# Performance work log

Measured on AMD Instinct MI355X. Metric: run time of the kernel, lower is better.

## Reference

```python
import jax, jax.numpy as jnp
import numpy as np

N = 10000
E = 160000
NEG_SLOPE = 0.2  # PyG GATConv default leaky_relu slope


def _gat_layer(x, src, dst, W, a_src, a_dst, b):
    """PyG GATConv with concat=True, add_self_loops=False.
    x: [N, Fin], W: [Fin, H*C], a_src/a_dst: [H, C], b: [H*C].
    """
    H, C = a_src.shape
    h = (x @ W).reshape(-1, H, C)                      # [N, H, C]
    al_s = jnp.sum(h * a_src, axis=-1)                 # [N, H]
    al_d = jnp.sum(h * a_dst, axis=-1)                 # [N, H]
    e = jax.nn.leaky_relu(al_s[src] + al_d[dst], NEG_SLOPE)  # [E, H]
    # segment softmax over edges grouped by destination node
    m = jax.ops.segment_max(e, dst, num_segments=N)    # [N, H]
    m = jnp.where(jnp.isfinite(m), m, 0.0)
    ex = jnp.exp(e - m[dst])                           # [E, H]
    den = jax.ops.segment_sum(ex, dst, num_segments=N)  # [N, H]
    alpha = ex / jnp.maximum(den[dst], 1e-16)          # [E, H]
    # scatter-add weighted source features
    out = jax.ops.segment_sum(alpha[:, :, None] * h[src], dst, num_segments=N)  # [N, H, C]
    return out.reshape(-1, H * C) + b


def setup_inputs() -> dict:
    key = jax.random.key(0)
    ks = jax.random.split(key, 16)
    s = 0.05
    return {
        "x": jax.random.normal(ks[0], (N, 300), jnp.float32),
        "edge_index": jax.random.randint(ks[1], (2, E), 0, N, jnp.int32),
        "W1": jax.random.normal(ks[2], (300, 512), jnp.float32) * s,
        "att_src1": jax.random.normal(ks[3], (4, 128), jnp.float32) * s,
        "att_dst1": jax.random.normal(ks[4], (4, 128), jnp.float32) * s,
        "b1": jax.random.normal(ks[5], (512,), jnp.float32) * s,
        "Wl1": jax.random.normal(ks[6], (300, 512), jnp.float32) * s,
        "bl1": jax.random.normal(ks[7], (512,), jnp.float32) * s,
        "W2": jax.random.normal(ks[8], (512, 2048), jnp.float32) * s,
        "att_src2": jax.random.normal(ks[9], (4, 512), jnp.float32) * s,
        "att_dst2": jax.random.normal(ks[10], (4, 512), jnp.float32) * s,
        "b2": jax.random.normal(ks[11], (2048,), jnp.float32) * s,
        "Wl2": jax.random.normal(ks[12], (512, 2048), jnp.float32) * s,
        "bl2": jax.random.normal(ks[13], (2048,), jnp.float32) * s,
    }


def reference(x, edge_index, W1, att_src1, att_dst1, b1, Wl1, bl1,
              W2, att_src2, att_dst2, b2, Wl2, bl2):
    src, dst = edge_index[0], edge_index[1]
    h1 = _gat_layer(x, src, dst, W1, att_src1, att_dst1, b1) + (x @ Wl1 + bl1)
    h1 = jax.nn.relu(h1)
    out = _gat_layer(h1, src, dst, W2, att_src2, att_dst2, b2) + (h1 @ Wl2 + bl2)
    return out
```

## Files before the change

### kernel.cpp

```cpp
#include <hip/hip_runtime.h>
#include <hip/hip_bf16.h>
#include <cstdint>


__device__ __forceinline__ float lrelu(float v) { return v >= 0.f ? v : 0.2f * v; }

__device__ __forceinline__ short f2bf(float x) {
  unsigned u = __float_as_uint(x);
  unsigned r = (u + 0x7fffu + ((u >> 16) & 1u)) >> 16;
  return (short)r;
}
__device__ __forceinline__ float bf2f(short b) {
  return __uint_as_float(((unsigned)(unsigned short)b) << 16);
}

typedef __attribute__((ext_vector_type(8))) short bf16x8;
typedef __attribute__((ext_vector_type(4))) float f32x4;

__device__ __forceinline__ void gload_lds16(const void* g, void* l) {
  auto gp = (const __attribute__((address_space(1))) unsigned int*)(uintptr_t)g;
  auto lp = (__attribute__((address_space(3))) unsigned int*)(uintptr_t)l;
  __builtin_amdgcn_global_load_lds(gp, lp, 16, 0, 0);
}

__global__ void count_edges_k(const int* __restrict__ dstv, int* __restrict__ counts, int E) {
  int e = blockIdx.x * 256 + threadIdx.x;
  if (e < E) atomicAdd(&counts[dstv[e]], 1);
}

__global__ void scan_k(const int* __restrict__ counts, int* __restrict__ rowptr,
                       int* __restrict__ cursor, int n) {
  __shared__ int wsum[16];
  __shared__ int s_base;
  int tid = threadIdx.x, lane = tid & 63, wv = tid >> 6;
  if (tid == 0) s_base = 0;
  __syncthreads();
  for (int base = 0; base < n; base += 1024) {
    int i = base + tid;
    int v = (i < n) ? counts[i] : 0;
    int x = v;
#pragma unroll
    for (int off = 1; off < 64; off <<= 1) {
      int t = __shfl_up(x, off);
      if (lane >= off) x += t;
    }
    if (lane == 63) wsum[wv] = x;
    __syncthreads();
    int woff = 0, tot = 0;
#pragma unroll
    for (int w = 0; w < 16; ++w) {
      int s = wsum[w];
      tot += s;
      if (w < wv) woff += s;
    }
    int b = s_base;
    if (i < n) {
      int excl = b + woff + x - v;
      rowptr[i] = excl;
      cursor[i] = excl;
    }
    __syncthreads();
    if (tid == 0) s_base = b + tot;
  }
  __syncthreads();
  if (tid == 0) rowptr[n] = s_base;
}

__global__ void fill_csr_k(const int* __restrict__ srcv, const int* __restrict__ dstv,
                           int* __restrict__ cursor, int* __restrict__ csr_src, int E) {
  int e = blockIdx.x * 256 + threadIdx.x;
  if (e < E) {
    int p = atomicAdd(&cursor[dstv[e]], 1);
    csr_src[p] = srcv[e];
  }
}

__global__ void xsplit_k(const float* __restrict__ x, short* __restrict__ xh,
                         short* __restrict__ xl, int total) {
  int idx = blockIdx.x * 256 + threadIdx.x;
  if (idx >= total) return;
  int n = idx / 320, k = idx - n * 320;
  float v = (k < 300) ? x[(size_t)n * 300 + k] : 0.f;
  short h = f2bf(v);
  xh[idx] = h;
  xl[idx] = f2bf(v - bf2f(h));
}

__global__ void wsplit_t_k(const float* __restrict__ W, short* __restrict__ Wth,
                           short* __restrict__ Wtl, int Nn, int Kin, int Kpad) {
  int idx = blockIdx.x * 256 + threadIdx.x;
  if (idx >= Nn * Kpad) return;
  int n = idx / Kpad, k = idx - n * Kpad;
  float a = (k < Kin) ? W[(size_t)k * Nn + n] : 0.f;
  short h = f2bf(a);
  Wth[idx] = h;
  Wtl[idx] = f2bf(a - bf2f(h));
}

template <bool BIAS>
__global__ __launch_bounds__(256) void gemm_bf16x3_k(
    const short* __restrict__ Ah, const short* __restrict__ Al,
    const short* __restrict__ Bh, const short* __restrict__ Bl,
    const float* __restrict__ bias, float* __restrict__ C,
    int M, int Nn, int K) {
  __shared__ __align__(16) short Ash[128 * 32];
  __shared__ __align__(16) short Asl[128 * 32];
  __shared__ __align__(16) short Bsh[128 * 32];
  __shared__ __align__(16) short Bsl[128 * 32];
  int tid = threadIdx.x, w = tid >> 6, l = tid & 63;
  int m0 = blockIdx.y * 128, n0 = blockIdx.x * 128;
  int wm = (w >> 1) * 64, wn = (w & 1) * 64;

  f32x4 acc[4][4] = {};

  int r_in = l >> 2;
  int kq = (l & 3) * 8;
  int arow_base = m0 + w * 32 + r_in;
  int brow_base = n0 + w * 32 + r_in;
  int lbase = (w * 32) * 32;

  int fr = l & 15, fk = (l >> 4) * 8;

  for (int k0 = 0; k0 < K; k0 += 32) {
    __syncthreads();
#pragma unroll
    for (int i = 0; i < 2; ++i) {
      int am = min(arow_base + i * 16, M - 1);
      int bn = brow_base + i * 16;
      size_t aoff = (size_t)am * K + k0 + kq;
      size_t boff = (size_t)bn * K + k0 + kq;
      int lofs = lbase + i * (16 * 32);
      gload_lds16(Ah + aoff, &Ash[lofs]);
      gload_lds16(Al + aoff, &Asl[lofs]);
      gload_lds16(Bh + boff, &Bsh[lofs]);
      gload_lds16(Bl + boff, &Bsl[lofs]);
    }
    __syncthreads();

    bf16x8 afh[4], afl[4], bfh[4], bfl[4];
#pragma unroll
    for (int t = 0; t < 4; ++t) {
      int ar = wm + t * 16 + fr;
      afh[t] = *(const bf16x8*)&Ash[ar * 32 + fk];
      afl[t] = *(const bf16x8*)&Asl[ar * 32 + fk];
      int br = wn + t * 16 + fr;
      bfh[t] = *(const bf16x8*)&Bsh[br * 32 + fk];
      bfl[t] = *(const bf16x8*)&Bsl[br * 32 + fk];
    }
#pragma unroll
    for (int mi = 0; mi < 4; ++mi)
#pragma unroll
      for (int ni = 0; ni < 4; ++ni) {
        acc[mi][ni] = __builtin_amdgcn_mfma_f32_16x16x32_bf16(afh[mi], bfh[ni], acc[mi][ni], 0, 0, 0);
        acc[mi][ni] = __builtin_amdgcn_mfma_f32_16x16x32_bf16(afh[mi], bfl[ni], acc[mi][ni], 0, 0, 0);
        acc[mi][ni] = __builtin_amdgcn_mfma_f32_16x16x32_bf16(afl[mi], bfh[ni], acc[mi][ni], 0, 0, 0);
      }
  }

  int fq = (l >> 4) * 4;
#pragma unroll
  for (int ni = 0; ni < 4; ++ni) {
    int gc = n0 + wn + ni * 16 + fr;
    float bv = BIAS ? bias[gc] : 0.f;
#pragma unroll
    for (int mi = 0; mi < 4; ++mi) {
      int grb = m0 + wm + mi * 16 + fq;
#pragma unroll
      for (int r = 0; r < 4; ++r) {
        int gr = grb + r;
        if (gr < M) C[(size_t)gr * Nn + gc] = acc[mi][ni][r] + bv;
      }
    }
  }
}

template <int C>
__global__ __launch_bounds__(256) void att_coef_k(
    const float* __restrict__ hfeat, const float* __restrict__ a_src,
    const float* __restrict__ a_dst, float* __restrict__ al_s,
    float* __restrict__ al_d, int n) {
  int wave = threadIdx.x >> 6, lane = threadIdx.x & 63;
  int node = blockIdx.x * 4 + wave;
  if (node >= n) return;
  constexpr int F = 4 * C;
  const float* hrow = hfeat + (size_t)node * F;
  float s[4] = {0, 0, 0, 0}, d[4] = {0, 0, 0, 0};
  for (int f = lane; f < F; f += 64) {
    float hv = hrow[f];
    int h = f / C;
    s[h] = fmaf(hv, a_src[f], s[h]);
    d[h] = fmaf(hv, a_dst[f], d[h]);
  }
#pragma unroll
  for (int off = 32; off; off >>= 1) {
#pragma unroll
    for (int h = 0; h < 4; ++h) {
      s[h] += __shfl_xor(s[h], off);
      d[h] += __shfl_xor(d[h], off);
    }
  }
  if (lane == 0) {
#pragma unroll
    for (int h = 0; h < 4; ++h) {
      al_s[node * 4 + h] = s[h];
      al_d[node * 4 + h] = d[h];
    }
  }
}

__global__ __launch_bounds__(256) void edge_alpha_k(
    const float* __restrict__ al_s, const float* __restrict__ al_d,
    const int* __restrict__ rowptr, const int* __restrict__ csr_src,
    float* __restrict__ alpha, int N) {
  int wave = threadIdx.x >> 6, lane = threadIdx.x & 63;
  int n = blockIdx.x * 4 + wave;
  if (n >= N) return;
  int r0 = rowptr[n], r1 = rowptr[n + 1];
  float ald[4];
#pragma unroll
  for (int h = 0; h < 4; ++h) ald[h] = al_d[n * 4 + h];

  float m[4] = {-3.4e38f, -3.4e38f, -3.4e38f, -3.4e38f};
  for (int e = r0 + lane; e < r1; e += 64) {
    int s = csr_src[e];
#pragma unroll
    for (int h = 0; h < 4; ++h) m[h] = fmaxf(m[h], lrelu(al_s[s * 4 + h] + ald[h]));
  }
#pragma unroll
  for (int off = 32; off; off >>= 1)
#pragma unroll
    for (int h = 0; h < 4; ++h) m[h] = fmaxf(m[h], __shfl_xor(m[h], off));

  float den[4] = {0, 0, 0, 0};
  for (int e = r0 + lane; e < r1; e += 64) {
    int s = csr_src[e];
#pragma unroll
    for (int h = 0; h < 4; ++h) den[h] += expf(lrelu(al_s[s * 4 + h] + ald[h]) - m[h]);
  }
#pragma unroll
  for (int off = 32; off; off >>= 1)
#pragma unroll
    for (int h = 0; h < 4; ++h) den[h] += __shfl_xor(den[h], off);

  float rden[4];
#pragma unroll
  for (int h = 0; h < 4; ++h) rden[h] = 1.f / fmaxf(den[h], 1e-16f);

  for (int e = r0 + lane; e < r1; e += 64) {
    int s = csr_src[e];
#pragma unroll
    for (int h = 0; h < 4; ++h)
      alpha[(size_t)e * 4 + h] = expf(lrelu(al_s[s * 4 + h] + ald[h]) - m[h]) * rden[h];
  }
}

template <int F, int TILE, bool RELU, bool SPLIT>
__global__ __launch_bounds__(256) void spmm_k(
    const float* __restrict__ hfeat, const float* __restrict__ alpha,
    const int* __restrict__ rowptr, const int* __restrict__ csr_src,
    const float* __restrict__ bias, const float* __restrict__ skip,
    float* __restrict__ out, short* __restrict__ oh, short* __restrict__ ol, int N) {
  constexpr int VE = TILE / 64;
  constexpr int C = F / 4;
  int wave = threadIdx.x >> 6, lane = threadIdx.x & 63;
  int n = blockIdx.x * 4 + wave;
  if (n >= N) return;
  int y = blockIdx.y;
  int col = y * TILE + lane * VE;
  int head = (y * TILE) / C;
  int r0 = rowptr[n], r1 = rowptr[n + 1];
  int len = r1 - r0;
  unsigned laneoff = (unsigned)(lane * VE);

  float acc[4][VE] = {};
  for (int base = 0; base < len; base += 64) {
    unsigned sj = 0;
    float aj = 0.f;
    if (base + lane < len) {
      int e = r0 + base + lane;
      sj = (unsigned)csr_src[e] * (unsigned)F + (unsigned)(y * TILE);
      aj = alpha[(size_t)e * 4 + head];
    }
    int cnt = min(64, len - base);
    int j = 0;
    for (; j + 4 <= cnt; j += 4) {
#pragma unroll
      for (int q = 0; q < 4; ++q) {
        unsigned sF = (unsigned)__builtin_amdgcn_readlane((int)sj, j + q);
        float a = __uint_as_float(
            (unsigned)__builtin_amdgcn_readlane((int)__float_as_uint(aj), j + q));
        const float* row = hfeat + sF;
        if (VE == 4) {
          float4 v = *(const float4*)(row + laneoff);
          acc[q][0] = fmaf(a, v.x, acc[q][0]);
          acc[q][1] = fmaf(a, v.y, acc[q][1]);
          acc[q][2] = fmaf(a, v.z, acc[q][2]);
          acc[q][3] = fmaf(a, v.w, acc[q][3]);
        } else {
          float2 v = *(const float2*)(row + laneoff);
          acc[q][0] = fmaf(a, v.x, acc[q][0]);
          acc[q][1] = fmaf(a, v.y, acc[q][1]);
        }
      }
    }
    for (; j < cnt; ++j) {
      unsigned sF = (unsigned)__builtin_amdgcn_readlane((int)sj, j);
      float a = __uint_as_float(
          (unsigned)__builtin_amdgcn_readlane((int)__float_as_uint(aj), j));
      const float* row = hfeat + sF;
      if (VE == 4) {
        float4 v = *(const float4*)(row + laneoff);
        acc[j & 3][0] = fmaf(a, v.x, acc[j & 3][0]);
        acc[j & 3][1] = fmaf(a, v.y, acc[j & 3][1]);
        acc[j & 3][2] = fmaf(a, v.z, acc[j & 3][2]);
        acc[j & 3][3] = fmaf(a, v.w, acc[j & 3][3]);
      } else {
        float2 v = *(const float2*)(row + laneoff);
        acc[j & 3][0] = fmaf(a, v.x, acc[j & 3][0]);
        acc[j & 3][1] = fmaf(a, v.y, acc[j & 3][1]);
      }
    }
  }

  size_t o = (size_t)n * F + col;
  float r[VE];
#pragma unroll
  for (int v = 0; v < VE; ++v)
    r[v] = ((acc[0][v] + acc[1][v]) + (acc[2][v] + acc[3][v])) +
           bias[col + v] + skip[o + v];
  if (RELU) {
#pragma unroll
    for (int v = 0; v < VE; ++v) r[v] = fmaxf(r[v], 0.f);
  }
  if (SPLIT) {
#pragma unroll
    for (int v = 0; v < VE; ++v) {
      short h = f2bf(r[v]);
      oh[o + v] = h;
      ol[o + v] = f2bf(r[v] - bf2f(h));
    }
  } else {
#pragma unroll
    for (int v = 0; v < VE; ++v) out[o + v] = r[v];
  }
}

extern "C" void kernel_launch(void* const* d_in, const int* in_sizes, int n_in,
                              void* d_out, int out_size, void* d_ws, size_t ws_size,
                              hipStream_t stream) {
  (void)n_in; (void)out_size; (void)ws_size;
  const float* x   = (const float*)d_in[0];
  const int*   ei  = (const int*)d_in[1];
  const float* W1  = (const float*)d_in[2];
  const float* as1 = (const float*)d_in[3];
  const float* ad1 = (const float*)d_in[4];
  const float* b1  = (const float*)d_in[5];
  const float* Wl1 = (const float*)d_in[6];
  const float* bl1 = (const float*)d_in[7];
  const float* W2  = (const float*)d_in[8];
  const float* as2 = (const float*)d_in[9];
  const float* ad2 = (const float*)d_in[10];
  const float* b2  = (const float*)d_in[11];
  const float* Wl2 = (const float*)d_in[12];
  const float* bl2 = (const float*)d_in[13];

  const int N = 10000;
  const int E = in_sizes[1] / 2;
  const int* srcv = ei;
  const int* dstv = ei + E;

  char* p = (char*)d_ws;
  float* hfeat = (float*)p; p += (size_t)N * 2048 * 4;
  float* s1 = hfeat + (size_t)N * 512;
  short* xh = (short*)(hfeat + (size_t)N * 1024);
  short* xl = xh + (size_t)N * 320;
  short* h1h = (short*)p; p += (size_t)N * 512 * 2;
  short* h1l = (short*)p; p += (size_t)N * 512 * 2;
  short* w2ht = (short*)p; p += (size_t)2048 * 512 * 2;
  short* w2lt = (short*)p; p += (size_t)2048 * 512 * 2;
  short* wl2ht = (short*)p; p += (size_t)2048 * 512 * 2;
  short* wl2lt = (short*)p; p += (size_t)2048 * 512 * 2;
  short* w1ht = (short*)p; p += (size_t)512 * 320 * 2;
  short* w1lt = (short*)p; p += (size_t)512 * 320 * 2;
  short* wl1ht = (short*)p; p += (size_t)512 * 320 * 2;
  short* wl1lt = (short*)p; p += (size_t)512 * 320 * 2;
  float* als = (float*)p; p += (size_t)N * 4 * 4;
  float* ald = (float*)p; p += (size_t)N * 4 * 4;
  float* alpha = (float*)p; p += (size_t)E * 4 * 4;
  int* rowptr = (int*)p; p += (N + 1) * 4;
  int* cursor = (int*)p; p += N * 4;
  int* counts = (int*)p; p += N * 4;
  int* csr_src = (int*)p; p += (size_t)E * 4;

  hipMemsetAsync(counts, 0, N * sizeof(int), stream);
  count_edges_k<<<(E + 255) / 256, 256, 0, stream>>>(dstv, counts, E);
  scan_k<<<1, 1024, 0, stream>>>(counts, rowptr, cursor, N);
  fill_csr_k<<<(E + 255) / 256, 256, 0, stream>>>(srcv, dstv, cursor, csr_src, E);

  xsplit_k<<<(N * 320 + 255) / 256, 256, 0, stream>>>(x, xh, xl, N * 320);
  wsplit_t_k<<<(512 * 320 + 255) / 256, 256, 0, stream>>>(W1, w1ht, w1lt, 512, 300, 320);
  wsplit_t_k<<<(512 * 320 + 255) / 256, 256, 0, stream>>>(Wl1, wl1ht, wl1lt, 512, 300, 320);
  wsplit_t_k<<<(2048 * 512 + 255) / 256, 256, 0, stream>>>(W2, w2ht, w2lt, 2048, 512, 512);
  wsplit_t_k<<<(2048 * 512 + 255) / 256, 256, 0, stream>>>(Wl2, wl2ht, wl2lt, 2048, 512, 512);

  gemm_bf16x3_k<false><<<dim3(512 / 128, (N + 127) / 128), 256, 0, stream>>>(
      xh, xl, w1ht, w1lt, nullptr, hfeat, N, 512, 320);
  gemm_bf16x3_k<true><<<dim3(512 / 128, (N + 127) / 128), 256, 0, stream>>>(
      xh, xl, wl1ht, wl1lt, bl1, s1, N, 512, 320);
  att_coef_k<128><<<(N + 3) / 4, 256, 0, stream>>>(hfeat, as1, ad1, als, ald, N);
  edge_alpha_k<<<(N + 3) / 4, 256, 0, stream>>>(als, ald, rowptr, csr_src, alpha, N);
  spmm_k<512, 128, true, true><<<dim3((N + 3) / 4, 512 / 128), 256, 0, stream>>>(
      hfeat, alpha, rowptr, csr_src, b1, s1, nullptr, h1h, h1l, N);

  gemm_bf16x3_k<false><<<dim3(2048 / 128, (N + 127) / 128), 256, 0, stream>>>(
      h1h, h1l, w2ht, w2lt, nullptr, hfeat, N, 2048, 512);
  gemm_bf16x3_k<true><<<dim3(2048 / 128, (N + 127) / 128), 256, 0, stream>>>(
      h1h, h1l, wl2ht, wl2lt, bl2, (float*)d_out, N, 2048, 512);
  att_coef_k<512><<<(N + 3) / 4, 256, 0, stream>>>(hfeat, as2, ad2, als, ald, N);
  edge_alpha_k<<<(N + 3) / 4, 256, 0, stream>>>(als, ald, rowptr, csr_src, alpha, N);
  spmm_k<2048, 256, false, false><<<dim3((N + 3) / 4, 2048 / 256), 256, 0, stream>>>(
      hfeat, alpha, rowptr, csr_src, b2, (float*)d_out, (float*)d_out, nullptr, nullptr, N);
}
```

Before: 631.3 us.

## Merge GAT and skip GEMMs into one launch, widen SpMM accumulators to eight

Concatenates the transposed split weights of the GAT projection and the linear skip path so each layer runs a single GEMM over the doubled output width, routing columns to the two destinations and adding the bias only on the skip half. This removes one kernel launch per layer and gives a larger grid for better occupancy and tail behaviour. The SpMM gather loop is also unrolled to eight independent accumulators to expose more outstanding loads per wave, at the cost of extra registers.

```diff
diff --git a/kernel.cpp b/kernel.cpp
--- a/kernel.cpp
+++ b/kernel.cpp
@@ -97,12 +97,11 @@
   Wtl[idx] = f2bf(a - bf2f(h));
 }
 
-template <bool BIAS>
 __global__ __launch_bounds__(256) void gemm_bf16x3_k(
     const short* __restrict__ Ah, const short* __restrict__ Al,
     const short* __restrict__ Bh, const short* __restrict__ Bl,
-    const float* __restrict__ bias, float* __restrict__ C,
-    int M, int Nn, int K) {
+    const float* __restrict__ bias2, float* __restrict__ C1, float* __restrict__ C2,
+    int M, int NS, int K) {
   __shared__ __align__(16) short Ash[128 * 32];
   __shared__ __align__(16) short Asl[128 * 32];
   __shared__ __align__(16) short Bsh[128 * 32];
@@ -161,14 +160,17 @@
 #pragma unroll
   for (int ni = 0; ni < 4; ++ni) {
     int gc = n0 + wn + ni * 16 + fr;
-    float bv = BIAS ? bias[gc] : 0.f;
+    bool second = gc >= NS;
+    float bv = second ? bias2[gc - NS] : 0.f;
+    float* Cp = second ? C2 : C1;
+    int cc = second ? gc - NS : gc;
 #pragma unroll
     for (int mi = 0; mi < 4; ++mi) {
       int grb = m0 + wm + mi * 16 + fq;
 #pragma unroll
       for (int r = 0; r < 4; ++r) {
         int gr = grb + r;
-        if (gr < M) C[(size_t)gr * Nn + gc] = acc[mi][ni][r] + bv;
+        if (gr < M) Cp[(size_t)gr * NS + cc] = acc[mi][ni][r] + bv;
       }
     }
   }
@@ -272,7 +274,7 @@
   int len = r1 - r0;
   unsigned laneoff = (unsigned)(lane * VE);
 
-  float acc[4][VE] = {};
+  float acc[8][VE] = {};
   for (int base = 0; base < len; base += 64) {
     unsigned sj = 0;
     float aj = 0.f;
@@ -283,9 +285,9 @@
     }
     int cnt = min(64, len - base);
     int j = 0;
-    for (; j + 4 <= cnt; j += 4) {
-#pragma unroll
-      for (int q = 0; q < 4; ++q) {
+    for (; j + 8 <= cnt; j += 8) {
+#pragma unroll
+      for (int q = 0; q < 8; ++q) {
         unsigned sF = (unsigned)__builtin_amdgcn_readlane((int)sj, j + q);
         float a = __uint_as_float(
             (unsigned)__builtin_amdgcn_readlane((int)__float_as_uint(aj), j + q));
@@ -310,14 +312,14 @@
       const float* row = hfeat + sF;
       if (VE == 4) {
         float4 v = *(const float4*)(row + laneoff);
-        acc[j & 3][0] = fmaf(a, v.x, acc[j & 3][0]);
-        acc[j & 3][1] = fmaf(a, v.y, acc[j & 3][1]);
-        acc[j & 3][2] = fmaf(a, v.z, acc[j & 3][2]);
-        acc[j & 3][3] = fmaf(a, v.w, acc[j & 3][3]);
+        acc[j & 7][0] = fmaf(a, v.x, acc[j & 7][0]);
+        acc[j & 7][1] = fmaf(a, v.y, acc[j & 7][1]);
+        acc[j & 7][2] = fmaf(a, v.z, acc[j & 7][2]);
+        acc[j & 7][3] = fmaf(a, v.w, acc[j & 7][3]);
       } else {
         float2 v = *(const float2*)(row + laneoff);
-        acc[j & 3][0] = fmaf(a, v.x, acc[j & 3][0]);
-        acc[j & 3][1] = fmaf(a, v.y, acc[j & 3][1]);
+        acc[j & 7][0] = fmaf(a, v.x, acc[j & 7][0]);
+        acc[j & 7][1] = fmaf(a, v.y, acc[j & 7][1]);
       }
     }
   }
@@ -326,7 +328,8 @@
   float r[VE];
 #pragma unroll
   for (int v = 0; v < VE; ++v)
-    r[v] = ((acc[0][v] + acc[1][v]) + (acc[2][v] + acc[3][v])) +
+    r[v] = (((acc[0][v] + acc[1][v]) + (acc[2][v] + acc[3][v])) +
+            ((acc[4][v] + acc[5][v]) + (acc[6][v] + acc[7][v]))) +
            bias[col + v] + skip[o + v];
   if (RELU) {
 #pragma unroll
@@ -376,14 +379,10 @@
   short* xl = xh + (size_t)N * 320;
   short* h1h = (short*)p; p += (size_t)N * 512 * 2;
   short* h1l = (short*)p; p += (size_t)N * 512 * 2;
-  short* w2ht = (short*)p; p += (size_t)2048 * 512 * 2;
-  short* w2lt = (short*)p; p += (size_t)2048 * 512 * 2;
-  short* wl2ht = (short*)p; p += (size_t)2048 * 512 * 2;
-  short* wl2lt = (short*)p; p += (size_t)2048 * 512 * 2;
-  short* w1ht = (short*)p; p += (size_t)512 * 320 * 2;
-  short* w1lt = (short*)p; p += (size_t)512 * 320 * 2;
-  short* wl1ht = (short*)p; p += (size_t)512 * 320 * 2;
-  short* wl1lt = (short*)p; p += (size_t)512 * 320 * 2;
+  short* w2cat_h = (short*)p; p += (size_t)4096 * 512 * 2;
+  short* w2cat_l = (short*)p; p += (size_t)4096 * 512 * 2;
+  short* w1cat_h = (short*)p; p += (size_t)1024 * 320 * 2;
+  short* w1cat_l = (short*)p; p += (size_t)1024 * 320 * 2;
   float* als = (float*)p; p += (size_t)N * 4 * 4;
   float* ald = (float*)p; p += (size_t)N * 4 * 4;
   float* alpha = (float*)p; p += (size_t)E * 4 * 4;
@@ -398,24 +397,22 @@
   fill_csr_k<<<(E + 255) / 256, 256, 0, stream>>>(srcv, dstv, cursor, csr_src, E);
 
   xsplit_k<<<(N * 320 + 255) / 256, 256, 0, stream>>>(x, xh, xl, N * 320);
-  wsplit_t_k<<<(512 * 320 + 255) / 256, 256, 0, stream>>>(W1, w1ht, w1lt, 512, 300, 320);
-  wsplit_t_k<<<(512 * 320 + 255) / 256, 256, 0, stream>>>(Wl1, wl1ht, wl1lt, 512, 300, 320);
-  wsplit_t_k<<<(2048 * 512 + 255) / 256, 256, 0, stream>>>(W2, w2ht, w2lt, 2048, 512, 512);
-  wsplit_t_k<<<(2048 * 512 + 255) / 256, 256, 0, stream>>>(Wl2, wl2ht, wl2lt, 2048, 512, 512);
-
-  gemm_bf16x3_k<false><<<dim3(512 / 128, (N + 127) / 128), 256, 0, stream>>>(
-      xh, xl, w1ht, w1lt, nullptr, hfeat, N, 512, 320);
-  gemm_bf16x3_k<true><<<dim3(512 / 128, (N + 127) / 128), 256, 0, stream>>>(
-      xh, xl, wl1ht, wl1lt, bl1, s1, N, 512, 320);
+  wsplit_t_k<<<(512 * 320 + 255) / 256, 256, 0, stream>>>(W1, w1cat_h, w1cat_l, 512, 300, 320);
+  wsplit_t_k<<<(512 * 320 + 255) / 256, 256, 0, stream>>>(
+      Wl1, w1cat_h + (size_t)512 * 320, w1cat_l + (size_t)512 * 320, 512, 300, 320);
+  wsplit_t_k<<<(2048 * 512 + 255) / 256, 256, 0, stream>>>(W2, w2cat_h, w2cat_l, 2048, 512, 512);
+  wsplit_t_k<<<(2048 * 512 + 255) / 256, 256, 0, stream>>>(
+      Wl2, w2cat_h + (size_t)2048 * 512, w2cat_l + (size_t)2048 * 512, 2048, 512, 512);
+
+  gemm_bf16x3_k<<<dim3(1024 / 128, (N + 127) / 128), 256, 0, stream>>>(
+      xh, xl, w1cat_h, w1cat_l, bl1, hfeat, s1, N, 512, 320);
   att_coef_k<128><<<(N + 3) / 4, 256, 0, stream>>>(hfeat, as1, ad1, als, ald, N);
   edge_alpha_k<<<(N + 3) / 4, 256, 0, stream>>>(als, ald, rowptr, csr_src, alpha, N);
   spmm_k<512, 128, true, true><<<dim3((N + 3) / 4, 512 / 128), 256, 0, stream>>>(
       hfeat, alpha, rowptr, csr_src, b1, s1, nullptr, h1h, h1l, N);
 
-  gemm_bf16x3_k<false><<<dim3(2048 / 128, (N + 127) / 128), 256, 0, stream>>>(
-      h1h, h1l, w2ht, w2lt, nullptr, hfeat, N, 2048, 512);
-  gemm_bf16x3_k<true><<<dim3(2048 / 128, (N + 127) / 128), 256, 0, stream>>>(
-      h1h, h1l, wl2ht, wl2lt, bl2, (float*)d_out, N, 2048, 512);
+  gemm_bf16x3_k<<<dim3(4096 / 128, (N + 127) / 128), 256, 0, stream>>>(
+      h1h, h1l, w2cat_h, w2cat_l, bl2, hfeat, (float*)d_out, N, 2048, 512);
   att_coef_k<512><<<(N + 3) / 4, 256, 0, stream>>>(hfeat, as2, ad2, als, ald, N);
   edge_alpha_k<<<(N + 3) / 4, 256, 0, stream>>>(als, ald, rowptr, csr_src, alpha, N);
   spmm_k<2048, 256, false, false><<<dim3((N + 3) / 4, 2048 / 256), 256, 0, stream>>>(
```

Measured after the change: 707.1 us. +12.0%, slower.
